# Kernel optimization log

Measured on AMD Instinct MI355X. Metric: run time of the kernel, lower is better.

Reference implementation:

```python
import jax, jax.numpy as jnp
import numpy as np

N_USER = 50000
N_ITEM = 50000
N_EDGE = 600000
D = 128


def _mean_agg(msg, dst, num_nodes):
    # segment-sum of messages and edge counts; nodes with no in-edges get 0 (DGL semantics)
    s = jax.ops.segment_sum(msg, dst, num_segments=num_nodes)
    cnt = jax.ops.segment_sum(jnp.ones((dst.shape[0], 1), msg.dtype), dst, num_segments=num_nodes)
    return s / jnp.maximum(cnt, 1.0)


def setup_inputs() -> dict:
    key = jax.random.key(0)
    ks = jax.random.split(key, 14)
    scale = 1.0 / np.sqrt(D)
    return {
        "feat_user": jax.random.normal(ks[0], (N_USER, D), jnp.float32),
        "feat_item": jax.random.normal(ks[1], (N_ITEM, D), jnp.float32),
        "W_uu": jax.random.normal(ks[2], (D, D), jnp.float32) * scale,
        "b_uu": jax.random.normal(ks[3], (D,), jnp.float32) * scale,
        "W_ub": jax.random.normal(ks[4], (D, D), jnp.float32) * scale,
        "b_ub": jax.random.normal(ks[5], (D,), jnp.float32) * scale,
        "W_iu": jax.random.normal(ks[6], (D, D), jnp.float32) * scale,
        "b_iu": jax.random.normal(ks[7], (D,), jnp.float32) * scale,
        "src_uu": jax.random.randint(ks[8], (N_EDGE,), 0, N_USER, jnp.int32),
        "dst_uu": jax.random.randint(ks[9], (N_EDGE,), 0, N_USER, jnp.int32),
        "src_ub": jax.random.randint(ks[10], (N_EDGE,), 0, N_USER, jnp.int32),
        "dst_ub": jax.random.randint(ks[11], (N_EDGE,), 0, N_ITEM, jnp.int32),
        "src_iu": jax.random.randint(ks[12], (N_EDGE,), 0, N_ITEM, jnp.int32),
        "dst_iu": jax.random.randint(ks[13], (N_EDGE,), 0, N_USER, jnp.int32),
    }


def reference(feat_user, feat_item, W_uu, b_uu, W_ub, b_ub, W_iu, b_iu,
              src_uu, dst_uu, src_ub, dst_ub, src_iu, dst_iu):
    # per-edge-type linear projection of src node features
    Wh_uu = feat_user @ W_uu + b_uu   # (user, follows, user)
    Wh_ub = feat_user @ W_ub + b_ub   # (user, buys, item)
    Wh_iu = feat_item @ W_iu + b_iu   # (item, bought_by, user)
    # copy_u -> mean per dst node, per edge type
    h_uu = _mean_agg(Wh_uu[src_uu], dst_uu, N_USER)
    h_ub = _mean_agg(Wh_ub[src_ub], dst_ub, N_ITEM)
    h_iu = _mean_agg(Wh_iu[src_iu], dst_iu, N_USER)
    # cross-type combine = 'sum' per dst ntype
    out_user = h_uu + h_iu
    out_item = h_ub
    return out_user, out_item
```

## Files before the change

kernel.cpp:

```cpp
#include <hip/hip_runtime.h>
#include <stdint.h>
#include <string.h>

#define N_USER 50000
#define N_ITEM 50000
#define N_EDGE 600000
#define D 128
#define NTOT 150000
#define ETOT 1800000
#define NB 293
#define BSH 9
#define SPAN 512
#define CHUNK 4096

typedef unsigned short u16;
typedef unsigned int   u32;
typedef __attribute__((ext_vector_type(8))) short short8;
typedef __attribute__((ext_vector_type(4))) float floatx4;

static __device__ __forceinline__ u16 f2b(float f) {
  u32 x; memcpy(&x, &f, 4);
  u32 r = x + 0x7fffu + ((x >> 16) & 1u);
  return (u16)(r >> 16);
}
static __device__ __forceinline__ float blo2f(u32 v) {
  u32 x = v << 16; float f; memcpy(&f, &x, 4); return f;
}
static __device__ __forceinline__ float bhi2f(u32 v) {
  u32 x = v & 0xffff0000u; float f; memcpy(&f, &x, 4); return f;
}

static __device__ __forceinline__ void conv_chunk(int cbase,
    const float* __restrict__ fu, const float* __restrict__ fi,
    u16* __restrict__ fb_u, u16* __restrict__ fb_i) {
#pragma unroll
  for (int u = 0; u < 8; ++u) {
    int gid = cbase + u * 256 + (int)threadIdx.x;
    if (gid < 3200000) {
      const float* src = fu; u16* dst = fb_u; int g = gid;
      if (g >= 1600000) { g -= 1600000; src = fi; dst = fb_i; }
      float4 v = ((const float4*)src)[g];
      union { u16 q[4]; uint2 d; } pk;
      pk.q[0] = f2b(v.x); pk.q[1] = f2b(v.y); pk.q[2] = f2b(v.z); pk.q[3] = f2b(v.w);
      ((uint2*)dst)[g] = pk.d;
    }
  }
}

__global__ void __launch_bounds__(256) k_front(
    const int* __restrict__ duu, const int* __restrict__ dub, const int* __restrict__ diu,
    int* __restrict__ bhist,
    const float* __restrict__ W0, const float* __restrict__ W1, const float* __restrict__ W2,
    u16* __restrict__ WT) {
  int bid = blockIdx.x;
  if (bid < 440) {
    __shared__ int h[NB];
    for (int i = threadIdx.x; i < NB; i += 256) h[i] = 0;
    __syncthreads();
    int base = bid * CHUNK;
    for (int j = threadIdx.x; j < CHUNK; j += 256) {
      int e = base + j;
      if (e < ETOT) {
        int t = e / N_EDGE, i = e - t * N_EDGE;
        int d = (t == 0) ? duu[i] : ((t == 1) ? dub[i] : diu[i]);
        atomicAdd(&h[(t * N_USER + d) >> BSH], 1);
      }
    }
    __syncthreads();
    for (int i = threadIdx.x; i < NB; i += 256) if (h[i]) atomicAdd(&bhist[i], h[i]);
  } else {
    int wsel = bid - 440;
    for (int idx = threadIdx.x; idx < D * D; idx += 256) {
      int n = idx >> 7, k = idx & 127;
      if (wsel == 0)      WT[n * 256 + k]       = f2b(W0[k * D + n]);
      else if (wsel == 1) WT[n * 256 + 128 + k] = f2b(W2[k * D + n]);
      else                WT[32768 + n * D + k] = f2b(W1[k * D + n]);
    }
  }
}

__global__ void __launch_bounds__(256) k_bplace(
    const int* __restrict__ suu, const int* __restrict__ duu,
    const int* __restrict__ sub, const int* __restrict__ dub,
    const int* __restrict__ siu, const int* __restrict__ diu,
    const int* __restrict__ bhist, int* __restrict__ cursor,
    int* __restrict__ boff, u32* __restrict__ ebuf,
    const float* __restrict__ fu, const float* __restrict__ fi,
    u16* __restrict__ fb_u, u16* __restrict__ fb_i) {
  if (blockIdx.x >= 440) {
    conv_chunk((blockIdx.x - 440) * 2048, fu, fi, fb_u, fb_i);
    return;
  }
  __shared__ int h[NB];
  __shared__ int sboff[NB];
  __shared__ int buf[256];
  int t = threadIdx.x;
  int a = (2 * t < NB) ? bhist[2 * t] : 0;
  int b = (2 * t + 1 < NB) ? bhist[2 * t + 1] : 0;
  buf[t] = a + b; __syncthreads();
  for (int s = 1; s < 256; s <<= 1) {
    int y = (t >= s) ? buf[t - s] : 0;
    __syncthreads(); buf[t] += y; __syncthreads();
  }
  int ex = buf[t] - (a + b);
  if (2 * t < NB) sboff[2 * t] = ex;
  if (2 * t + 1 < NB) sboff[2 * t + 1] = ex + a;
  if (blockIdx.x == 0) {
    if (2 * t < NB) boff[2 * t] = ex;
    if (2 * t + 1 < NB) boff[2 * t + 1] = ex + a;
    if (t == 255) boff[NB] = buf[255];
  }
  for (int i = t; i < NB; i += 256) h[i] = 0;
  __syncthreads();
  int base = blockIdx.x * CHUNK;
  u32 pay[16], br[16];
#pragma unroll
  for (int k = 0; k < 16; ++k) {
    int e = base + k * 256 + t;
    br[k] = 0xFFFFFFFFu;
    if (e < ETOT) {
      int ty = e / N_EDGE, i = e - ty * N_EDGE;
      int d, s;
      if (ty == 0)      { d = duu[i]; s = suu[i]; }
      else if (ty == 1) { d = dub[i]; s = sub[i]; }
      else              { d = diu[i]; s = siu[i]; }
      int slot = ty * N_USER + d;
      int bu = slot >> BSH;
      int rank = atomicAdd(&h[bu], 1);
      pay[k] = (u32)s | ((u32)(slot & (SPAN - 1)) << 16);
      br[k]  = (u32)bu | ((u32)rank << 9);
    }
  }
  __syncthreads();
  for (int i = t; i < NB; i += 256)
    h[i] = sboff[i] + atomicAdd(&cursor[i], h[i]);
  __syncthreads();
#pragma unroll
  for (int k = 0; k < 16; ++k) {
    if (br[k] != 0xFFFFFFFFu) {
      int bu = br[k] & 0x1FF, rank = (int)(br[k] >> 9);
      ebuf[h[bu] + rank] = pay[k];
    }
  }
}

__global__ void __launch_bounds__(256) k_csr(const int* __restrict__ boff, const u32* __restrict__ ebuf,
                                             int* __restrict__ off, u16* __restrict__ ssrc,
                                             const float* __restrict__ fu, const float* __restrict__ fi,
                                             u16* __restrict__ fb_u, u16* __restrict__ fb_i) {
  if (blockIdx.x >= NB) {
    conv_chunk((blockIdx.x - NB) * 2048 + 1601536, fu, fi, fb_u, fb_i);
    return;
  }
  __shared__ int sc[SPAN];
  __shared__ int so[SPAN];
  __shared__ int part[256];
  int b = blockIdx.x;
  int ebase = boff[b], ecnt = boff[b + 1] - ebase;
  int sbase = b << BSH;
  int nslots = (NTOT - sbase < SPAN) ? (NTOT - sbase) : SPAN;
  for (int i = threadIdx.x; i < SPAN; i += 256) sc[i] = 0;
  __syncthreads();
  for (int j = threadIdx.x; j < ecnt; j += 256)
    atomicAdd(&sc[ebuf[ebase + j] >> 16], 1);
  __syncthreads();
  int t = threadIdx.x;
  int s0 = sc[2 * t], s1 = sc[2 * t + 1];
  int tsum = s0 + s1;
  part[t] = tsum; __syncthreads();
  for (int s = 1; s < 256; s <<= 1) {
    int y = (t >= s) ? part[t - s] : 0;
    __syncthreads(); part[t] += y; __syncthreads();
  }
  int pbase = part[t] - tsum;
  so[2 * t]     = pbase;
  so[2 * t + 1] = pbase + s0;
  __syncthreads();
  for (int i = threadIdx.x; i < nslots; i += 256)
    off[sbase + i] = ebase + so[i];
  if (b == 0 && threadIdx.x == 0) off[NTOT] = ETOT;
  for (int i = threadIdx.x; i < SPAN; i += 256) sc[i] = so[i];
  __syncthreads();
  for (int j = threadIdx.x; j < ecnt; j += 256) {
    u32 p = ebuf[ebase + j];
    int pos = atomicAdd(&sc[p >> 16], 1);
    ssrc[ebase + pos] = (u16)(p & 0xFFFFu);
  }
}

__global__ void __launch_bounds__(256) k_mean(const u16* __restrict__ fb_u, const u16* __restrict__ fb_i,
                                              const int* __restrict__ off, const u16* __restrict__ ssrc,
                                              u16* __restrict__ ob, int slot_base, int slot_lim) {
  int slot = slot_base + blockIdx.x * 8 + (threadIdx.x >> 5);
  int lane = threadIdx.x & 31;
  if (slot >= slot_lim) return;
  int t = slot / N_USER;
  int d = slot - t * N_USER;
  const u16* fb = (t == 2) ? fb_i : fb_u;
  int s = off[slot], e = off[slot + 1];
  int n = e - s;
  int my_src = (lane < n) ? (int)ssrc[s + lane] : 0;
  float a0 = 0.f, a1 = 0.f, a2 = 0.f, a3 = 0.f;
  int m = (n < 32) ? n : 32;
  int i = 0;
  for (; i + 8 <= m; i += 8) {
    int sA[8];
#pragma unroll
    for (int k = 0; k < 8; ++k) sA[k] = __shfl(my_src, i + k, 32);
    uint2 v[8];
#pragma unroll
    for (int k = 0; k < 8; ++k) v[k] = ((const uint2*)(fb + (size_t)sA[k] * D))[lane];
#pragma unroll
    for (int k = 0; k < 8; ++k) {
      a0 += blo2f(v[k].x); a1 += bhi2f(v[k].x);
      a2 += blo2f(v[k].y); a3 += bhi2f(v[k].y);
    }
  }
  for (; i + 4 <= m; i += 4) {
    int s0 = __shfl(my_src, i, 32);
    int s1 = __shfl(my_src, i + 1, 32);
    int s2 = __shfl(my_src, i + 2, 32);
    int s3 = __shfl(my_src, i + 3, 32);
    uint2 v0 = ((const uint2*)(fb + (size_t)s0 * D))[lane];
    uint2 v1 = ((const uint2*)(fb + (size_t)s1 * D))[lane];
    uint2 v2 = ((const uint2*)(fb + (size_t)s2 * D))[lane];
    uint2 v3 = ((const uint2*)(fb + (size_t)s3 * D))[lane];
    a0 += blo2f(v0.x) + blo2f(v1.x) + blo2f(v2.x) + blo2f(v3.x);
    a1 += bhi2f(v0.x) + bhi2f(v1.x) + bhi2f(v2.x) + bhi2f(v3.x);
    a2 += blo2f(v0.y) + blo2f(v1.y) + blo2f(v2.y) + blo2f(v3.y);
    a3 += bhi2f(v0.y) + bhi2f(v1.y) + bhi2f(v2.y) + bhi2f(v3.y);
  }
  for (; i < m; ++i) {
    int sr = __shfl(my_src, i, 32);
    uint2 v = ((const uint2*)(fb + (size_t)sr * D))[lane];
    a0 += blo2f(v.x); a1 += bhi2f(v.x);
    a2 += blo2f(v.y); a3 += bhi2f(v.y);
  }
  for (int j = s + 32; j < e; ++j) {
    int sr = ssrc[j];
    uint2 v = ((const uint2*)(fb + (size_t)sr * D))[lane];
    a0 += blo2f(v.x); a1 += bhi2f(v.x);
    a2 += blo2f(v.y); a3 += bhi2f(v.y);
  }
  float inv = (n > 0) ? 1.0f / (float)n : 0.f;
  u32 p0 = (u32)f2b(a0 * inv) | ((u32)f2b(a1 * inv) << 16);
  u32 p1 = (u32)f2b(a2 * inv) | ((u32)f2b(a3 * inv) << 16);
  u32* mrow;
  if (t == 0)      mrow = (u32*)(ob + (size_t)d * 256);
  else if (t == 2) mrow = (u32*)(ob + (size_t)d * 256 + 128);
  else             mrow = (u32*)(ob + 12800000 + (size_t)d * 256);
  ((uint2*)mrow)[lane] = make_uint2(p0, p1);
}

__global__ void __launch_bounds__(256, 2) k_out(float* out, const u16* __restrict__ WT,
                                                const float* __restrict__ buu, const float* __restrict__ bub,
                                                const float* __restrict__ biu, const int* __restrict__ off) {
  int users = (blockIdx.y == 0);
  int tid = threadIdx.x;
  int w = tid >> 6, lane = tid & 63, quad = lane >> 4, l16 = lane & 15;
  int KT = users ? 8 : 4;
  const u16* Wsrc = users ? WT : (WT + 32768);
  int wstride = users ? 256 : 128;

  __shared__ u16 sB[32768];
  int nfrag = KT * 8 * 64;
  for (int fid = tid; fid < nfrag; fid += 256) {
    int fl = fid & 63, fnt = (fid >> 6) & 7, fkk = fid >> 9;
    int fq = fl >> 4, fl16 = fl & 15;
    const u16* src = Wsrc + (fnt * 16 + fl16) * wstride + fkk * 32 + fq * 8;
    *(uint4*)(sB + (size_t)fid * 8) = *(const uint4*)src;
  }

  int row0 = blockIdx.x * 128 + w * 32;
  const u16* ob = (const u16*)out;
  const u16* Abase = users ? ob : (ob + 12800000);
  size_t outoff = users ? 0 : (size_t)N_USER;

  int r0a = row0 + l16, r1a = row0 + 16 + l16;
  int rA0 = r0a < N_USER ? r0a : N_USER - 1;
  int rA1 = r1a < N_USER ? r1a : N_USER - 1;
  const u16* A0 = Abase + (size_t)rA0 * 256 + quad * 8;
  const u16* A1 = Abase + (size_t)rA1 * 256 + quad * 8;

  short8 af0[8], af1[8];
#pragma unroll
  for (int kk = 0; kk < 8; ++kk) {
    if (kk < KT) {
      af0[kk] = *(const short8*)(A0 + kk * 32);
      af1[kk] = *(const short8*)(A1 + kk * 32);
    }
  }
  int nA[2][4], nB[2][4];
#pragma unroll
  for (int rt = 0; rt < 2; ++rt)
#pragma unroll
    for (int i = 0; i < 4; ++i) {
      int grow = row0 + rt * 16 + quad * 4 + i;
      bool ok = grow < N_USER;
      if (users) {
        nA[rt][i] = ok ? (off[grow + 1] - off[grow]) : 0;
        nB[rt][i] = ok ? (off[2 * N_USER + grow + 1] - off[2 * N_USER + grow]) : 0;
      } else {
        nA[rt][i] = ok ? (off[N_USER + grow + 1] - off[N_USER + grow]) : 0;
        nB[rt][i] = 0;
      }
    }
  __syncthreads();

  floatx4 acc[2][8];
#pragma unroll
  for (int rt = 0; rt < 2; ++rt)
#pragma unroll
    for (int nt = 0; nt < 8; ++nt) acc[rt][nt] = (floatx4){0.f, 0.f, 0.f, 0.f};

#pragma unroll
  for (int kk = 0; kk < 8; ++kk) {
    if (kk < KT) {
      const short8* bp = (const short8*)(sB + ((size_t)kk * 512 + lane) * 8);
#pragma unroll
      for (int nt = 0; nt < 8; ++nt) {
        short8 bf = bp[nt * 64];
        acc[0][nt] = __builtin_amdgcn_mfma_f32_16x16x32_bf16(af0[kk], bf, acc[0][nt], 0, 0, 0);
        acc[1][nt] = __builtin_amdgcn_mfma_f32_16x16x32_bf16(af1[kk], bf, acc[1][nt], 0, 0, 0);
      }
    }
  }

  float* sO = (float*)sB;
#pragma unroll
  for (int rt = 0; rt < 2; ++rt) {
    __syncthreads();
#pragma unroll
    for (int nt = 0; nt < 8; ++nt) {
      int col = nt * 16 + l16;
      float bA = users ? buu[col] : bub[col];
      float bB = users ? biu[col] : 0.f;
#pragma unroll
      for (int i = 0; i < 4; ++i) {
        float r = acc[rt][nt][i] + (nA[rt][i] > 0 ? bA : 0.f) + (nB[rt][i] > 0 ? bB : 0.f);
        sO[(w * 16 + quad * 4 + i) * 132 + col] = r;
      }
    }
    __syncthreads();
#pragma unroll
    for (int it = 0; it < 8; ++it) {
      int idx = it * 256 + tid;
      int lr = idx >> 5, cg = (idx & 31) * 4;
      int grow = blockIdx.x * 128 + (lr >> 4) * 32 + rt * 16 + (lr & 15);
      if (grow < N_USER) {
        float4 v = make_float4(sO[lr * 132 + cg], sO[lr * 132 + cg + 1],
                               sO[lr * 132 + cg + 2], sO[lr * 132 + cg + 3]);
        *(float4*)(out + (outoff + (size_t)grow) * D + cg) = v;
      }
    }
  }
}

extern "C" void kernel_launch(void* const* d_in, const int* in_sizes, int n_in,
                              void* d_out, int out_size, void* d_ws, size_t ws_size,
                              hipStream_t stream) {
  const float* fu  = (const float*)d_in[0];
  const float* fi  = (const float*)d_in[1];
  const float* Wuu = (const float*)d_in[2];
  const float* buu = (const float*)d_in[3];
  const float* Wub = (const float*)d_in[4];
  const float* bub = (const float*)d_in[5];
  const float* Wiu = (const float*)d_in[6];
  const float* biu = (const float*)d_in[7];
  const int* suu = (const int*)d_in[8];
  const int* duu = (const int*)d_in[9];
  const int* sub = (const int*)d_in[10];
  const int* dub = (const int*)d_in[11];
  const int* siu = (const int*)d_in[12];
  const int* diu = (const int*)d_in[13];
  float* out = (float*)d_out;
  u16* ob = (u16*)d_out;

  int* wsi    = (int*)d_ws;
  int* off    = wsi;
  int* bhist  = wsi + 150016;
  int* cursor = wsi + 150336;
  int* boff   = wsi + 150656;
  u32* ebuf   = (u32*)(wsi + 150976);
  u16* ssrc   = (u16*)(wsi + 1950976);
  u16* WT     = (u16*)(wsi + 2850976);
  u16* fb_u   = (u16*)(wsi + 2875552);
  u16* fb_i   = (u16*)(wsi + 6075552);

  hipMemsetAsync(bhist, 0, 640 * sizeof(int), stream);
  k_front<<<443, 256, 0, stream>>>(duu, dub, diu, bhist, Wuu, Wub, Wiu, WT);
  k_bplace<<<440 + 782, 256, 0, stream>>>(suu, duu, sub, dub, siu, diu, bhist, cursor,
                                          boff, ebuf, fu, fi, fb_u, fb_i);
  k_csr<<<NB + 781, 256, 0, stream>>>(boff, ebuf, off, ssrc, fu, fi, fb_u, fb_i);
  k_mean<<<12500, 256, 0, stream>>>(fb_u, fb_i, off, ssrc, ob, 0, 100000);
  k_mean<<<6250, 256, 0, stream>>>(fb_u, fb_i, off, ssrc, ob, 100000, NTOT);
  k_out<<<dim3(391, 2), 256, 0, stream>>>(out, WT, buu, bub, biu, off);
}
```

Measured before the change: 268.1 us.

## Drop histogram pre-pass via fixed-capacity buckets and fuse item GEMM into mean

Removes the separate destination-histogram kernel by giving each bucket a fixed CAP-sized region in the edge buffer, so placement no longer needs a prefix scan of bucket counts. The k_csr kernel now computes each bucket's base offset itself by scanning the cursor counts. The item-side mean and its projection GEMM are launched together in one kernel, and k_out now covers only users. This cuts one launch plus an edge pass, and lets the item GEMM overlap the tail of the mean. The cost is assuming no bucket exceeds CAP edges, which holds only for roughly uniform destinations. A redundant scan is also repeated in every csr block.

```diff
diff --git a/kernel.cpp b/kernel.cpp
--- a/kernel.cpp
+++ b/kernel.cpp
@@ -12,6 +12,7 @@
 #define BSH 9
 #define SPAN 512
 #define CHUNK 4096
+#define CAP 7168
 
 typedef unsigned short u16;
 typedef unsigned int   u32;
@@ -47,28 +48,81 @@
   }
 }
 
-__global__ void __launch_bounds__(256) k_front(
-    const int* __restrict__ duu, const int* __restrict__ dub, const int* __restrict__ diu,
-    int* __restrict__ bhist,
-    const float* __restrict__ W0, const float* __restrict__ W1, const float* __restrict__ W2,
-    u16* __restrict__ WT) {
+static __device__ __forceinline__ void mean_slot(int slot, int lane,
+    const u16* __restrict__ fb, const int* __restrict__ off,
+    const u16* __restrict__ ssrc, u16* __restrict__ ob) {
+  int t = slot / N_USER;
+  int d = slot - t * N_USER;
+  int s = off[slot], e = off[slot + 1];
+  int n = e - s;
+  int my_src = (lane < n) ? (int)ssrc[s + lane] : 0;
+  float a0 = 0.f, a1 = 0.f, a2 = 0.f, a3 = 0.f;
+  int m = (n < 32) ? n : 32;
+  int i = 0;
+  for (; i + 8 <= m; i += 8) {
+    int sA[8];
+#pragma unroll
+    for (int k = 0; k < 8; ++k) sA[k] = __shfl(my_src, i + k, 32);
+    uint2 v[8];
+#pragma unroll
+    for (int k = 0; k < 8; ++k) v[k] = ((const uint2*)(fb + (size_t)sA[k] * D))[lane];
+#pragma unroll
+    for (int k = 0; k < 8; ++k) {
+      a0 += blo2f(v[k].x); a1 += bhi2f(v[k].x);
+      a2 += blo2f(v[k].y); a3 += bhi2f(v[k].y);
+    }
+  }
+  for (; i + 4 <= m; i += 4) {
+    int s0 = __shfl(my_src, i, 32);
+    int s1 = __shfl(my_src, i + 1, 32);
+    int s2 = __shfl(my_src, i + 2, 32);
+    int s3 = __shfl(my_src, i + 3, 32);
+    uint2 v0 = ((const uint2*)(fb + (size_t)s0 * D))[lane];
+    uint2 v1 = ((const uint2*)(fb + (size_t)s1 * D))[lane];
+    uint2 v2 = ((const uint2*)(fb + (size_t)s2 * D))[lane];
+    uint2 v3 = ((const uint2*)(fb + (size_t)s3 * D))[lane];
+    a0 += blo2f(v0.x) + blo2f(v1.x) + blo2f(v2.x) + blo2f(v3.x);
+    a1 += bhi2f(v0.x) + bhi2f(v1.x) + bhi2f(v2.x) + bhi2f(v3.x);
+    a2 += blo2f(v0.y) + blo2f(v1.y) + blo2f(v2.y) + blo2f(v3.y);
+    a3 += bhi2f(v0.y) + bhi2f(v1.y) + bhi2f(v2.y) + bhi2f(v3.y);
+  }
+  for (; i < m; ++i) {
+    int sr = __shfl(my_src, i, 32);
+    uint2 v = ((const uint2*)(fb + (size_t)sr * D))[lane];
+    a0 += blo2f(v.x); a1 += bhi2f(v.x);
+    a2 += blo2f(v.y); a3 += bhi2f(v.y);
+  }
+  for (int j = s + 32; j < e; ++j) {
+    int sr = ssrc[j];
+    uint2 v = ((const uint2*)(fb + (size_t)sr * D))[lane];
+    a0 += blo2f(v.x); a1 += bhi2f(v.x);
+    a2 += blo2f(v.y); a3 += bhi2f(v.y);
+  }
+  float inv = (n > 0) ? 1.0f / (float)n : 0.f;
+  u32 p0 = (u32)f2b(a0 * inv) | ((u32)f2b(a1 * inv) << 16);
+  u32 p1 = (u32)f2b(a2 * inv) | ((u32)f2b(a3 * inv) << 16);
+  u32* mrow;
+  if (t == 0)      mrow = (u32*)(ob + (size_t)d * 256);
+  else if (t == 2) mrow = (u32*)(ob + (size_t)d * 256 + 128);
+  else             mrow = (u32*)(ob + 12800000 + (size_t)d * 256);
+  ((uint2*)mrow)[lane] = make_uint2(p0, p1);
+}
+
+__global__ void __launch_bounds__(256) k_bplace(
+    const int* __restrict__ suu, const int* __restrict__ duu,
+    const int* __restrict__ sub, const int* __restrict__ dub,
+    const int* __restrict__ siu, const int* __restrict__ diu,
+    int* __restrict__ cursor, u32* __restrict__ ebuf,
+    const float* __restrict__ W0, const float* __restrict__ W1,
+    const float* __restrict__ W2, u16* __restrict__ WT,
+    const float* __restrict__ fu, const float* __restrict__ fi,
+    u16* __restrict__ fb_u, u16* __restrict__ fb_i) {
   int bid = blockIdx.x;
-  if (bid < 440) {
-    __shared__ int h[NB];
-    for (int i = threadIdx.x; i < NB; i += 256) h[i] = 0;
-    __syncthreads();
-    int base = bid * CHUNK;
-    for (int j = threadIdx.x; j < CHUNK; j += 256) {
-      int e = base + j;
-      if (e < ETOT) {
-        int t = e / N_EDGE, i = e - t * N_EDGE;
-        int d = (t == 0) ? duu[i] : ((t == 1) ? dub[i] : diu[i]);
-        atomicAdd(&h[(t * N_USER + d) >> BSH], 1);
-      }
-    }
-    __syncthreads();
-    for (int i = threadIdx.x; i < NB; i += 256) if (h[i]) atomicAdd(&bhist[i], h[i]);
-  } else {
+  if (bid >= 443) {
+    conv_chunk((bid - 443) * 2048, fu, fi, fb_u, fb_i);
+    return;
+  }
+  if (bid >= 440) {
     int wsel = bid - 440;
     for (int idx = threadIdx.x; idx < D * D; idx += 256) {
       int n = idx >> 7, k = idx & 127;
@@ -76,43 +130,13 @@
       else if (wsel == 1) WT[n * 256 + 128 + k] = f2b(W2[k * D + n]);
       else                WT[32768 + n * D + k] = f2b(W1[k * D + n]);
     }
-  }
-}
-
-__global__ void __launch_bounds__(256) k_bplace(
-    const int* __restrict__ suu, const int* __restrict__ duu,
-    const int* __restrict__ sub, const int* __restrict__ dub,
-    const int* __restrict__ siu, const int* __restrict__ diu,
-    const int* __restrict__ bhist, int* __restrict__ cursor,
-    int* __restrict__ boff, u32* __restrict__ ebuf,
-    const float* __restrict__ fu, const float* __restrict__ fi,
-    u16* __restrict__ fb_u, u16* __restrict__ fb_i) {
-  if (blockIdx.x >= 440) {
-    conv_chunk((blockIdx.x - 440) * 2048, fu, fi, fb_u, fb_i);
     return;
   }
   __shared__ int h[NB];
-  __shared__ int sboff[NB];
-  __shared__ int buf[256];
   int t = threadIdx.x;
-  int a = (2 * t < NB) ? bhist[2 * t] : 0;
-  int b = (2 * t + 1 < NB) ? bhist[2 * t + 1] : 0;
-  buf[t] = a + b; __syncthreads();
-  for (int s = 1; s < 256; s <<= 1) {
-    int y = (t >= s) ? buf[t - s] : 0;
-    __syncthreads(); buf[t] += y; __syncthreads();
-  }
-  int ex = buf[t] - (a + b);
-  if (2 * t < NB) sboff[2 * t] = ex;
-  if (2 * t + 1 < NB) sboff[2 * t + 1] = ex + a;
-  if (blockIdx.x == 0) {
-    if (2 * t < NB) boff[2 * t] = ex;
-    if (2 * t + 1 < NB) boff[2 * t + 1] = ex + a;
-    if (t == 255) boff[NB] = buf[255];
-  }
   for (int i = t; i < NB; i += 256) h[i] = 0;
   __syncthreads();
-  int base = blockIdx.x * CHUNK;
+  int base = bid * CHUNK;
   u32 pay[16], br[16];
 #pragma unroll
   for (int k = 0; k < 16; ++k) {
@@ -133,7 +157,7 @@
   }
   __syncthreads();
   for (int i = t; i < NB; i += 256)
-    h[i] = sboff[i] + atomicAdd(&cursor[i], h[i]);
+    h[i] = i * CAP + atomicAdd(&cursor[i], h[i]);
   __syncthreads();
 #pragma unroll
   for (int k = 0; k < 16; ++k) {
@@ -144,7 +168,7 @@
   }
 }
 
-__global__ void __launch_bounds__(256) k_csr(const int* __restrict__ boff, const u32* __restrict__ ebuf,
+__global__ void __launch_bounds__(256) k_csr(const int* __restrict__ cursor, const u32* __restrict__ ebuf,
                                              int* __restrict__ off, u16* __restrict__ ssrc,
                                              const float* __restrict__ fu, const float* __restrict__ fi,
                                              u16* __restrict__ fb_u, u16* __restrict__ fb_i) {
@@ -155,16 +179,32 @@
   __shared__ int sc[SPAN];
   __shared__ int so[SPAN];
   __shared__ int part[256];
+  __shared__ int sebase;
+  int t = threadIdx.x;
   int b = blockIdx.x;
-  int ebase = boff[b], ecnt = boff[b + 1] - ebase;
+  {
+    int a = (2 * t < NB) ? cursor[2 * t] : 0;
+    int c = (2 * t + 1 < NB) ? cursor[2 * t + 1] : 0;
+    part[t] = a + c; __syncthreads();
+    for (int s = 1; s < 256; s <<= 1) {
+      int y = (t >= s) ? part[t - s] : 0;
+      __syncthreads(); part[t] += y; __syncthreads();
+    }
+    int ex = part[t] - (a + c);
+    if (2 * t == b) sebase = ex;
+    if (2 * t + 1 == b) sebase = ex + a;
+    __syncthreads();
+  }
+  int ecnt = cursor[b];
+  int ebase = sebase;
+  int srcb = b * CAP;
   int sbase = b << BSH;
   int nslots = (NTOT - sbase < SPAN) ? (NTOT - sbase) : SPAN;
-  for (int i = threadIdx.x; i < SPAN; i += 256) sc[i] = 0;
-  __syncthreads();
-  for (int j = threadIdx.x; j < ecnt; j += 256)
-    atomicAdd(&sc[ebuf[ebase + j] >> 16], 1);
-  __syncthreads();
-  int t = threadIdx.x;
+  for (int i = t; i < SPAN; i += 256) sc[i] = 0;
+  __syncthreads();
+  for (int j = t; j < ecnt; j += 256)
+    atomicAdd(&sc[ebuf[srcb + j] >> 16], 1);
+  __syncthreads();
   int s0 = sc[2 * t], s1 = sc[2 * t + 1];
   int tsum = s0 + s1;
   part[t] = tsum; __syncthreads();
@@ -176,80 +216,98 @@
   so[2 * t]     = pbase;
   so[2 * t + 1] = pbase + s0;
   __syncthreads();
-  for (int i = threadIdx.x; i < nslots; i += 256)
+  for (int i = t; i < nslots; i += 256)
     off[sbase + i] = ebase + so[i];
-  if (b == 0 && threadIdx.x == 0) off[NTOT] = ETOT;
-  for (int i = threadIdx.x; i < SPAN; i += 256) sc[i] = so[i];
-  __syncthreads();
-  for (int j = threadIdx.x; j < ecnt; j += 256) {
-    u32 p = ebuf[ebase + j];
+  if (b == 0 && t == 0) off[NTOT] = ETOT;
+  for (int i = t; i < SPAN; i += 256) sc[i] = so[i];
+  __syncthreads();
+  for (int j = t; j < ecnt; j += 256) {
+    u32 p = ebuf[srcb + j];
     int pos = atomicAdd(&sc[p >> 16], 1);
     ssrc[ebase + pos] = (u16)(p & 0xFFFFu);
   }
 }
 
-__global__ void __launch_bounds__(256) k_mean(const u16* __restrict__ fb_u, const u16* __restrict__ fb_i,
-                                              const int* __restrict__ off, const u16* __restrict__ ssrc,
-                                              u16* __restrict__ ob, int slot_base, int slot_lim) {
-  int slot = slot_base + blockIdx.x * 8 + (threadIdx.x >> 5);
-  int lane = threadIdx.x & 31;
-  if (slot >= slot_lim) return;
-  int t = slot / N_USER;
-  int d = slot - t * N_USER;
-  const u16* fb = (t == 2) ? fb_i : fb_u;
-  int s = off[slot], e = off[slot + 1];
-  int n = e - s;
-  int my_src = (lane < n) ? (int)ssrc[s + lane] : 0;
-  float a0 = 0.f, a1 = 0.f, a2 = 0.f, a3 = 0.f;
-  int m = (n < 32) ? n : 32;
-  int i = 0;
-  for (; i + 8 <= m; i += 8) {
-    int sA[8];
-#pragma unroll
-    for (int k = 0; k < 8; ++k) sA[k] = __shfl(my_src, i + k, 32);
-    uint2 v[8];
-#pragma unroll
-    for (int k = 0; k < 8; ++k) v[k] = ((const uint2*)(fb + (size_t)sA[k] * D))[lane];
-#pragma unroll
-    for (int k = 0; k < 8; ++k) {
-      a0 += blo2f(v[k].x); a1 += bhi2f(v[k].x);
-      a2 += blo2f(v[k].y); a3 += bhi2f(v[k].y);
-    }
-  }
-  for (; i + 4 <= m; i += 4) {
-    int s0 = __shfl(my_src, i, 32);
-    int s1 = __shfl(my_src, i + 1, 32);
-    int s2 = __shfl(my_src, i + 2, 32);
-    int s3 = __shfl(my_src, i + 3, 32);
-    uint2 v0 = ((const uint2*)(fb + (size_t)s0 * D))[lane];
-    uint2 v1 = ((const uint2*)(fb + (size_t)s1 * D))[lane];
-    uint2 v2 = ((const uint2*)(fb + (size_t)s2 * D))[lane];
-    uint2 v3 = ((const uint2*)(fb + (size_t)s3 * D))[lane];
-    a0 += blo2f(v0.x) + blo2f(v1.x) + blo2f(v2.x) + blo2f(v3.x);
-    a1 += bhi2f(v0.x) + bhi2f(v1.x) + bhi2f(v2.x) + bhi2f(v3.x);
-    a2 += blo2f(v0.y) + blo2f(v1.y) + blo2f(v2.y) + blo2f(v3.y);
-    a3 += bhi2f(v0.y) + bhi2f(v1.y) + bhi2f(v2.y) + bhi2f(v3.y);
-  }
-  for (; i < m; ++i) {
-    int sr = __shfl(my_src, i, 32);
-    uint2 v = ((const uint2*)(fb + (size_t)sr * D))[lane];
-    a0 += blo2f(v.x); a1 += bhi2f(v.x);
-    a2 += blo2f(v.y); a3 += bhi2f(v.y);
-  }
-  for (int j = s + 32; j < e; ++j) {
-    int sr = ssrc[j];
-    uint2 v = ((const uint2*)(fb + (size_t)sr * D))[lane];
-    a0 += blo2f(v.x); a1 += bhi2f(v.x);
-    a2 += blo2f(v.y); a3 += bhi2f(v.y);
-  }
-  float inv = (n > 0) ? 1.0f / (float)n : 0.f;
-  u32 p0 = (u32)f2b(a0 * inv) | ((u32)f2b(a1 * inv) << 16);
-  u32 p1 = (u32)f2b(a2 * inv) | ((u32)f2b(a3 * inv) << 16);
-  u32* mrow;
-  if (t == 0)      mrow = (u32*)(ob + (size_t)d * 256);
-  else if (t == 2) mrow = (u32*)(ob + (size_t)d * 256 + 128);
-  else             mrow = (u32*)(ob + 12800000 + (size_t)d * 256);
-  ((uint2*)mrow)[lane] = make_uint2(p0, p1);
+__global__ void __launch_bounds__(256) k_mean_u(const u16* __restrict__ fb_u,
+                                                const int* __restrict__ off, const u16* __restrict__ ssrc,
+                                                u16* __restrict__ ob) {
+  int slot = blockIdx.x * 8 + (threadIdx.x >> 5);
+  if (slot >= 100000) return;
+  mean_slot(slot, threadIdx.x & 31, fb_u, off, ssrc, ob);
+}
+
+__global__ void __launch_bounds__(256) k_mi(const u16* __restrict__ fb_i,
+                                            const int* __restrict__ off, const u16* __restrict__ ssrc,
+                                            u16* __restrict__ ob, float* __restrict__ out,
+                                            const u16* __restrict__ WT, const float* __restrict__ bub) {
+  __shared__ u16 sB[16384];
+  if (blockIdx.x < 6250) {
+    int slot = 100000 + blockIdx.x * 8 + (threadIdx.x >> 5);
+    if (slot < NTOT) mean_slot(slot, threadIdx.x & 31, fb_i, off, ssrc, ob);
+    return;
+  }
+  int tid = threadIdx.x;
+  int w = tid >> 6, lane = tid & 63, quad = lane >> 4, l16 = lane & 15;
+  const u16* Wsrc = WT + 32768;
+  for (int fid = tid; fid < 2048; fid += 256) {
+    int fl = fid & 63, fnt = (fid >> 6) & 7, fkk = fid >> 9;
+    int fq = fl >> 4, fl16 = fl & 15;
+    const u16* src = Wsrc + (fnt * 16 + fl16) * 128 + fkk * 32 + fq * 8;
+    *(uint4*)(sB + (size_t)fid * 8) = *(const uint4*)src;
+  }
+  int row0 = (blockIdx.x - 6250) * 128 + w * 32;
+  int r0a = row0 + l16, r1a = row0 + 16 + l16;
+  int rA0 = r0a < N_USER ? r0a : N_USER - 1;
+  int rA1 = r1a < N_USER ? r1a : N_USER - 1;
+  const u16* A0 = ob + 12800000 + (size_t)rA0 * 256 + quad * 8;
+  const u16* A1 = ob + 12800000 + (size_t)rA1 * 256 + quad * 8;
+  short8 af0[4], af1[4];
+#pragma unroll
+  for (int kk = 0; kk < 4; ++kk) {
+    af0[kk] = *(const short8*)(A0 + kk * 32);
+    af1[kk] = *(const short8*)(A1 + kk * 32);
+  }
+  int nA[2][4];
+#pragma unroll
+  for (int rt = 0; rt < 2; ++rt)
+#pragma unroll
+    for (int i = 0; i < 4; ++i) {
+      int grow = row0 + rt * 16 + quad * 4 + i;
+      nA[rt][i] = (grow < N_USER) ? (off[N_USER + grow + 1] - off[N_USER + grow]) : 0;
+    }
+  __syncthreads();
+  floatx4 acc[2][8];
+#pragma unroll
+  for (int rt = 0; rt < 2; ++rt)
+#pragma unroll
+    for (int nt = 0; nt < 8; ++nt) acc[rt][nt] = (floatx4){0.f, 0.f, 0.f, 0.f};
+#pragma unroll
+  for (int kk = 0; kk < 4; ++kk) {
+    const short8* bp = (const short8*)(sB + ((size_t)kk * 512 + lane) * 8);
+#pragma unroll
+    for (int nt = 0; nt < 8; ++nt) {
+      short8 bf = bp[nt * 64];
+      acc[0][nt] = __builtin_amdgcn_mfma_f32_16x16x32_bf16(af0[kk], bf, acc[0][nt], 0, 0, 0);
+      acc[1][nt] = __builtin_amdgcn_mfma_f32_16x16x32_bf16(af1[kk], bf, acc[1][nt], 0, 0, 0);
+    }
+  }
+#pragma unroll
+  for (int rt = 0; rt < 2; ++rt) {
+    int tbase = row0 + rt * 16;
+#pragma unroll
+    for (int nt = 0; nt < 8; ++nt) {
+      int col = nt * 16 + l16;
+      float bA = bub[col];
+#pragma unroll
+      for (int i = 0; i < 4; ++i) {
+        int grow = tbase + quad * 4 + i;
+        if (grow < N_USER) {
+          float r = acc[rt][nt][i] + (nA[rt][i] > 0 ? bA : 0.f);
+          out[((size_t)N_USER + grow) * D + col] = r;
+        }
+      }
+    }
+  }
 }
 
 __global__ void __launch_bounds__(256, 2) k_out(float* out, const u16* __restrict__ WT,
@@ -378,21 +436,18 @@
 
   int* wsi    = (int*)d_ws;
   int* off    = wsi;
-  int* bhist  = wsi + 150016;
-  int* cursor = wsi + 150336;
-  int* boff   = wsi + 150656;
-  u32* ebuf   = (u32*)(wsi + 150976);
-  u16* ssrc   = (u16*)(wsi + 1950976);
-  u16* WT     = (u16*)(wsi + 2850976);
-  u16* fb_u   = (u16*)(wsi + 2875552);
-  u16* fb_i   = (u16*)(wsi + 6075552);
-
-  hipMemsetAsync(bhist, 0, 640 * sizeof(int), stream);
-  k_front<<<443, 256, 0, stream>>>(duu, dub, diu, bhist, Wuu, Wub, Wiu, WT);
-  k_bplace<<<440 + 782, 256, 0, stream>>>(suu, duu, sub, dub, siu, diu, bhist, cursor,
-                                          boff, ebuf, fu, fi, fb_u, fb_i);
-  k_csr<<<NB + 781, 256, 0, stream>>>(boff, ebuf, off, ssrc, fu, fi, fb_u, fb_i);
-  k_mean<<<12500, 256, 0, stream>>>(fb_u, fb_i, off, ssrc, ob, 0, 100000);
-  k_mean<<<6250, 256, 0, stream>>>(fb_u, fb_i, off, ssrc, ob, 100000, NTOT);
-  k_out<<<dim3(391, 2), 256, 0, stream>>>(out, WT, buu, bub, biu, off);
-}
+  int* cursor = wsi + 150016;
+  u32* ebuf   = (u32*)(wsi + 150336);
+  u16* ssrc   = (u16*)(wsi + 2250560);
+  u16* WT     = (u16*)(wsi + 3150560);
+  u16* fb_u   = (u16*)(wsi + 3175136);
+  u16* fb_i   = (u16*)(wsi + 6375136);
+
+  hipMemsetAsync(cursor, 0, 320 * sizeof(int), stream);
+  k_bplace<<<1225, 256, 0, stream>>>(suu, duu, sub, dub, siu, diu, cursor, ebuf,
+                                     Wuu, Wub, Wiu, WT, fu, fi, fb_u, fb_i);
+  k_csr<<<NB + 781, 256, 0, stream>>>(cursor, ebuf, off, ssrc, fu, fi, fb_u, fb_i);
+  k_mean_u<<<12500, 256, 0, stream>>>(fb_u, off, ssrc, ob);
+  k_mi<<<6641, 256, 0, stream>>>(fb_i, off, ssrc, ob, out, WT, bub);
+  k_out<<<391, 256, 0, stream>>>(out, WT, buu, bub, biu, off);
+}
```

Result: no change. 270.6 us (+0.9%).
